# Optimization experiments

Hardware: AMD Instinct MI355X
Metric: run time of the kernel (lower is better)

Reference implementation:

```python
import jax, jax.numpy as jnp
import numpy as np

IN_F = 4096
OUT_F = 11008
BATCH = 4
SEQ = 2048


def setup_inputs() -> dict:
    key = jax.random.key(0)
    kx, kw, ks = jax.random.split(key, 3)
    x = jax.random.normal(kx, (BATCH, SEQ, IN_F), dtype=jnp.float32)
    # simulated int4 weights stored in an int container, range [0, 16)
    W_q = jax.random.randint(kw, (OUT_F, IN_F), 0, 16, dtype=jnp.int32)
    scale = jax.random.uniform(ks, (OUT_F,), dtype=jnp.float32)
    return {"x": x, "W_q": W_q, "scale": scale}


def reference(x, W_q, scale):
    # dequantize: per-output-channel scale, then y = x @ W_fp^T
    W_fp = W_q.astype(jnp.float32) * scale[:, None]  # [out, in]
    return jnp.einsum('bsi,oi->bso', x, W_fp)
```

## Files before the change

### kernel.cpp

```cpp
#include <hip/hip_runtime.h>
#include <math.h>

#define M_DIM 8192
#define N_DIM 11008
#define K_DIM 4096

#define BM 256
#define BN 128
#define BKB 64
#define NT (K_DIM / BKB)
#define NBN (N_DIM / BN)
#define NWG ((M_DIM / BM) * NBN)

#define BUF_STRIDE 24576
#define B_OFF 16384

typedef int int4v __attribute__((ext_vector_type(4)));
typedef int int16v __attribute__((ext_vector_type(16)));

__device__ __forceinline__ void async_copy16(const void* g, void* l) {
  __builtin_amdgcn_global_load_lds(
      (const __attribute__((address_space(1))) void*)g,
      (__attribute__((address_space(3))) void*)l, 16, 0, 0);
}

__global__ __launch_bounds__(256) void quant_x(const float* __restrict__ x,
                                               signed char* __restrict__ xq,
                                               float* __restrict__ sx) {
  __shared__ float wred[4];
  const int row = blockIdx.x;
  const int tid = threadIdx.x;
  const float4* src = (const float4*)(x + (size_t)row * K_DIM) + tid * 4;
  float4 v0 = src[0], v1 = src[1], v2 = src[2], v3 = src[3];

  float m = 0.f;
#define MX4(V) m = fmaxf(m, fmaxf(fmaxf(fabsf(V.x), fabsf(V.y)), fmaxf(fabsf(V.z), fabsf(V.w))))
  MX4(v0); MX4(v1); MX4(v2); MX4(v3);
#undef MX4
#pragma unroll
  for (int off = 32; off >= 1; off >>= 1)
    m = fmaxf(m, __shfl_xor(m, off, 64));
  if ((tid & 63) == 0) wred[tid >> 6] = m;
  __syncthreads();
  float smax = fmaxf(fmaxf(wred[0], wred[1]), fmaxf(wred[2], wred[3]));
  smax = fmaxf(smax, 1e-20f);
  const float inv = 127.f / smax;

  int4v o;
#define Q4(V, G) o[G] = ((int)rintf(V.x * inv) & 255) | (((int)rintf(V.y * inv) & 255) << 8) | \
                        (((int)rintf(V.z * inv) & 255) << 16) | (((int)rintf(V.w * inv) & 255) << 24)
  Q4(v0, 0); Q4(v1, 1); Q4(v2, 2); Q4(v3, 3);
#undef Q4
  ((int4v*)(xq + (size_t)row * K_DIM))[tid] = o;
  if (tid == 0) sx[row] = smax / 127.f;
}

__global__ __launch_bounds__(256) void pack_w(const int* __restrict__ in,
                                              signed char* __restrict__ wq) {
  const int idx = blockIdx.x * 256 + threadIdx.x;
  const int4* in4 = (const int4*)in + (size_t)idx * 4;
  int4 a = in4[0], b = in4[1], c = in4[2], d = in4[3];
  int4v o;
  o[0] = a.x | (a.y << 8) | (a.z << 16) | (a.w << 24);
  o[1] = b.x | (b.y << 8) | (b.z << 16) | (b.w << 24);
  o[2] = c.x | (c.y << 8) | (c.z << 16) | (c.w << 24);
  o[3] = d.x | (d.y << 8) | (d.z << 16) | (d.w << 24);
  ((int4v*)wq)[idx] = o;
}

__device__ __forceinline__ void stage_q(const signed char* __restrict__ P,
                                        int grow0, int k0b, char* dest, int tid) {
  const int rl = tid >> 2;
  const int key = ((rl >> 1) ^ (rl >> 3)) & 3;
  const int kb = (((tid & 3) ^ key) << 4);
  async_copy16(&P[(size_t)(grow0 + rl) * K_DIM + k0b + kb], dest + tid * 16);
}

__global__ __launch_bounds__(512, 4) void gemm_i8(
    const signed char* __restrict__ A, const signed char* __restrict__ B,
    const float* __restrict__ scale, const float* __restrict__ sx,
    float* __restrict__ out) {
  __shared__ __align__(16) char smw[2 * BUF_STRIDE];
  const int tid = threadIdx.x;
  const int lane = tid & 63;
  const int wv = tid >> 6;
  const int wr = wv >> 1, wc = wv & 1;
  const int l31 = lane & 31;
  const int h = lane >> 5;
  const int swz = ((((l31 >> 1) ^ (l31 >> 3)) & 3) << 4);

  int id = blockIdx.x;
  id = (id & 7) * (NWG / 8) + (id >> 3);
  const int bn = (id % NBN) * BN;
  const int bm = (id / NBN) * BM;

  int16v acc[2][2] = {};

  stage_q(A, bm,       0, smw,          tid);
  stage_q(A, bm + 128, 0, smw +  8192,  tid);
  stage_q(B, bn,       0, smw + B_OFF,  tid);
  asm volatile("s_waitcnt vmcnt(0)" ::: "memory");
  __builtin_amdgcn_s_barrier();

#pragma unroll 1
  for (int t = 0; t < NT; ++t) {
    const int cur = t & 1;
    const char* Abuf = smw + cur * BUF_STRIDE;
    const char* Bbuf = Abuf + B_OFF;
    char* nb = smw + (cur ^ 1) * BUF_STRIDE;
    const int k1 = (t + 1) * BKB;
    const bool pf = (t + 1 < NT);

#pragma unroll
    for (int kq = 0; kq < 2; ++kq) {
      const int cb = ((kq * 2 + h) << 4) ^ swz;
      int4v af[2], bfr[2];
#pragma unroll
      for (int mi = 0; mi < 2; ++mi)
        af[mi] = *(const int4v*)(Abuf + (wr * 64 + mi * 32 + l31) * 64 + cb);
#pragma unroll
      for (int ni = 0; ni < 2; ++ni)
        bfr[ni] = *(const int4v*)(Bbuf + (wc * 64 + ni * 32 + l31) * 64 + cb);
      if (pf) {
        if (kq == 0) {
          stage_q(A, bm,       k1, nb,        tid);
          stage_q(A, bm + 128, k1, nb + 8192, tid);
        } else {
          stage_q(B, bn,       k1, nb + B_OFF, tid);
        }
      }
      __builtin_amdgcn_s_setprio(1);
#pragma unroll
      for (int mi = 0; mi < 2; ++mi)
#pragma unroll
        for (int ni = 0; ni < 2; ++ni)
          acc[mi][ni] = __builtin_amdgcn_mfma_i32_32x32x32_i8(
              af[mi], bfr[ni], acc[mi][ni], 0, 0, 0);
      __builtin_amdgcn_s_setprio(0);
    }

    if (pf) {
      asm volatile("s_waitcnt vmcnt(0)" ::: "memory");
      __builtin_amdgcn_s_barrier();
    }
  }

  const int ocol0 = bn + wc * 64 + l31;
  const int orow0 = bm + wr * 64 + 4 * h;
#pragma unroll
  for (int ni = 0; ni < 2; ++ni) {
    const float sc = scale[ocol0 + ni * 32];
#pragma unroll
    for (int mi = 0; mi < 2; ++mi) {
#pragma unroll
      for (int reg = 0; reg < 16; ++reg) {
        const int row = orow0 + mi * 32 + (reg & 3) + 8 * (reg >> 2);
        out[(size_t)row * N_DIM + ocol0 + ni * 32] =
            (float)acc[mi][ni][reg] * sx[row] * sc;
      }
    }
  }
}

__global__ __launch_bounds__(256) void gemm_fallback(
    const float* __restrict__ X, const int* __restrict__ Wq,
    const float* __restrict__ scale, float* __restrict__ out) {
  __shared__ float Xs[64][17];
  __shared__ float Ws[64][17];
  const int tid = threadIdx.x;
  const int tn = blockIdx.x % (N_DIM / 64);
  const int tm = blockIdx.x / (N_DIM / 64);
  const int tr = tid >> 4, tc = tid & 15;
  float acc[4][4] = {};
  for (int k0 = 0; k0 < K_DIM; k0 += 16) {
#pragma unroll
    for (int i = 0; i < 4; ++i) {
      int idx = tid + i * 256;
      int r = idx >> 4, c = idx & 15;
      Xs[r][c] = X[(size_t)(tm * 64 + r) * K_DIM + k0 + c];
      Ws[r][c] = (float)Wq[(size_t)(tn * 64 + r) * K_DIM + k0 + c];
    }
    __syncthreads();
#pragma unroll
    for (int kk = 0; kk < 16; ++kk)
#pragma unroll
      for (int i = 0; i < 4; ++i) {
        float a = Xs[tr * 4 + i][kk];
#pragma unroll
        for (int j = 0; j < 4; ++j) acc[i][j] += a * Ws[tc * 4 + j][kk];
      }
    __syncthreads();
  }
#pragma unroll
  for (int i = 0; i < 4; ++i)
#pragma unroll
    for (int j = 0; j < 4; ++j) {
      int row = tm * 64 + tr * 4 + i, col = tn * 64 + tc * 4 + j;
      out[(size_t)row * N_DIM + col] = acc[i][j] * scale[col];
    }
}

extern "C" void kernel_launch(void* const* d_in, const int* in_sizes, int n_in,
                              void* d_out, int out_size, void* d_ws, size_t ws_size,
                              hipStream_t stream) {
  const float* x = (const float*)d_in[0];
  const int* Wq = (const int*)d_in[1];
  const float* scale = (const float*)d_in[2];
  float* out = (float*)d_out;

  const size_t XN = (size_t)M_DIM * K_DIM;
  const size_t WN = (size_t)N_DIM * K_DIM;
  const size_t need = XN + WN + M_DIM * sizeof(float);

  if (ws_size >= need) {
    signed char* xq = (signed char*)d_ws;
    signed char* wq = xq + XN;
    float* sx = (float*)(wq + WN);
    quant_x<<<M_DIM, 256, 0, stream>>>(x, xq, sx);
    pack_w<<<(unsigned)(WN / 4096), 256, 0, stream>>>(Wq, wq);
    gemm_i8<<<NWG, 512, 0, stream>>>(xq, wq, scale, sx, out);
  } else {
    gemm_fallback<<<(N_DIM / 64) * (M_DIM / 64), 256, 0, stream>>>(x, Wq, scale, out);
  }
}
```

Measured before the change: 497.8 us.

## Double K tile depth and switch the int8 GEMM to a single LDS buffer

Raises the K tile from 64 to 128 bytes, which halves the number of main-loop iterations and barriers. It replaces the double-buffered prefetch with a single shared buffer that is loaded, waited on and then consumed each iteration, and uses a new XOR swizzle for 128-byte rows. The occupancy hint drops from 4 to 2 blocks per CU, giving each thread more register room. The cost is that global loads no longer overlap MFMA work inside a block, so latency hiding now depends on other resident blocks.

```diff
diff --git a/kernel.cpp b/kernel.cpp
--- a/kernel.cpp
+++ b/kernel.cpp
@@ -7,13 +7,12 @@
 
 #define BM 256
 #define BN 128
-#define BKB 64
+#define BKB 128
 #define NT (K_DIM / BKB)
 #define NBN (N_DIM / BN)
 #define NWG ((M_DIM / BM) * NBN)
 
-#define BUF_STRIDE 24576
-#define B_OFF 16384
+#define B_OFF 32768
 
 typedef int int4v __attribute__((ext_vector_type(4)));
 typedef int int16v __attribute__((ext_vector_type(16)));
@@ -68,26 +67,26 @@
   ((int4v*)wq)[idx] = o;
 }
 
-__device__ __forceinline__ void stage_q(const signed char* __restrict__ P,
+__device__ __forceinline__ void stage_g(const signed char* __restrict__ P,
                                         int grow0, int k0b, char* dest, int tid) {
-  const int rl = tid >> 2;
-  const int key = ((rl >> 1) ^ (rl >> 3)) & 3;
-  const int kb = (((tid & 3) ^ key) << 4);
-  async_copy16(&P[(size_t)(grow0 + rl) * K_DIM + k0b + kb], dest + tid * 16);
-}
-
-__global__ __launch_bounds__(512, 4) void gemm_i8(
+  const int r = tid >> 3;
+  const int key = (r & 7) ^ ((tid >> 7) & 1);
+  const int c = (tid & 7) ^ key;
+  async_copy16(&P[(size_t)(grow0 + r) * K_DIM + k0b + c * 16], dest + tid * 16);
+}
+
+__global__ __launch_bounds__(512, 2) void gemm_i8(
     const signed char* __restrict__ A, const signed char* __restrict__ B,
     const float* __restrict__ scale, const float* __restrict__ sx,
     float* __restrict__ out) {
-  __shared__ __align__(16) char smw[2 * BUF_STRIDE];
+  __shared__ __align__(16) char smw[49152];
   const int tid = threadIdx.x;
   const int lane = tid & 63;
   const int wv = tid >> 6;
   const int wr = wv >> 1, wc = wv & 1;
   const int l31 = lane & 31;
   const int h = lane >> 5;
-  const int swz = ((((l31 >> 1) ^ (l31 >> 3)) & 3) << 4);
+  const int swz = (l31 & 7) ^ ((l31 >> 4) & 1);
 
   int id = blockIdx.x;
   id = (id & 7) * (NWG / 8) + (id >> 3);
@@ -96,39 +95,29 @@
 
   int16v acc[2][2] = {};
 
-  stage_q(A, bm,       0, smw,          tid);
-  stage_q(A, bm + 128, 0, smw +  8192,  tid);
-  stage_q(B, bn,       0, smw + B_OFF,  tid);
-  asm volatile("s_waitcnt vmcnt(0)" ::: "memory");
-  __builtin_amdgcn_s_barrier();
-
 #pragma unroll 1
   for (int t = 0; t < NT; ++t) {
-    const int cur = t & 1;
-    const char* Abuf = smw + cur * BUF_STRIDE;
-    const char* Bbuf = Abuf + B_OFF;
-    char* nb = smw + (cur ^ 1) * BUF_STRIDE;
-    const int k1 = (t + 1) * BKB;
-    const bool pf = (t + 1 < NT);
-
-#pragma unroll
-    for (int kq = 0; kq < 2; ++kq) {
-      const int cb = ((kq * 2 + h) << 4) ^ swz;
+    const int kb = t * BKB;
+    __builtin_amdgcn_s_barrier();
+    stage_g(A, bm,       kb, smw,         tid);
+    stage_g(A, bm + 64,  kb, smw +  8192, tid);
+    stage_g(A, bm + 128, kb, smw + 16384, tid);
+    stage_g(A, bm + 192, kb, smw + 24576, tid);
+    stage_g(B, bn,       kb, smw + B_OFF,        tid);
+    stage_g(B, bn + 64,  kb, smw + B_OFF + 8192, tid);
+    asm volatile("s_waitcnt vmcnt(0)" ::: "memory");
+    __builtin_amdgcn_s_barrier();
+
+#pragma unroll
+    for (int ks = 0; ks < 4; ++ks) {
+      const int cb = ((2 * ks + h) ^ swz) * 16;
       int4v af[2], bfr[2];
 #pragma unroll
       for (int mi = 0; mi < 2; ++mi)
-        af[mi] = *(const int4v*)(Abuf + (wr * 64 + mi * 32 + l31) * 64 + cb);
+        af[mi] = *(const int4v*)(smw + (wr * 64 + mi * 32 + l31) * 128 + cb);
 #pragma unroll
       for (int ni = 0; ni < 2; ++ni)
-        bfr[ni] = *(const int4v*)(Bbuf + (wc * 64 + ni * 32 + l31) * 64 + cb);
-      if (pf) {
-        if (kq == 0) {
-          stage_q(A, bm,       k1, nb,        tid);
-          stage_q(A, bm + 128, k1, nb + 8192, tid);
-        } else {
-          stage_q(B, bn,       k1, nb + B_OFF, tid);
-        }
-      }
+        bfr[ni] = *(const int4v*)(smw + B_OFF + (wc * 64 + ni * 32 + l31) * 128 + cb);
       __builtin_amdgcn_s_setprio(1);
 #pragma unroll
       for (int mi = 0; mi < 2; ++mi)
@@ -137,11 +126,6 @@
           acc[mi][ni] = __builtin_amdgcn_mfma_i32_32x32x32_i8(
               af[mi], bfr[ni], acc[mi][ni], 0, 0, 0);
       __builtin_amdgcn_s_setprio(0);
-    }
-
-    if (pf) {
-      asm volatile("s_waitcnt vmcnt(0)" ::: "memory");
-      __builtin_amdgcn_s_barrier();
     }
   }
 
```

After: 494.0 us. No clear change (-0.8%).
